# Kernel tuning notes

Measured on AMD Instinct MI355X. Metric: run time of the kernel, lower is better.

## Reference

```python
import jax, jax.numpy as jnp
import numpy as np


def _gcn_conv(x, W, b, src, dst, n):
    # PyG GCNConv: add self-loops, symmetric normalization deg^{-1/2} A deg^{-1/2},
    # linear transform, scatter-add aggregation, bias.
    h = x @ W  # [N, H]
    # degree including self-loop (count of dst occurrences + 1)
    deg = jnp.zeros((n,), h.dtype).at[dst].add(1.0) + 1.0
    dinv = jax.lax.rsqrt(deg)  # deg^{-1/2}
    edge_norm = (dinv[src] * dinv[dst])[:, None]  # [E, 1]
    agg = jax.ops.segment_sum(h[src] * edge_norm, dst, num_segments=n)  # [N, H]
    # self-loop contribution: norm = dinv[i]*dinv[i]
    return agg + h * (dinv * dinv)[:, None] + b


def setup_inputs() -> dict:
    N, E, F_IN, HID, OUT = 100000, 1600000, 128, 128, 64
    key = jax.random.key(0)
    ks = jax.random.split(key, 8)
    x = jax.random.normal(ks[0], (N, F_IN), dtype=jnp.float32)
    edge_index = jax.random.randint(ks[1], (2, E), 0, N, dtype=jnp.int32)
    s1 = 1.0 / np.sqrt(F_IN)
    s2 = 1.0 / np.sqrt(HID)
    W1 = jax.random.uniform(ks[2], (F_IN, HID), jnp.float32, -s1, s1)
    b1 = jax.random.uniform(ks[3], (HID,), jnp.float32, -s1, s1)
    W2 = jax.random.uniform(ks[4], (HID, HID), jnp.float32, -s2, s2)
    b2 = jax.random.uniform(ks[5], (HID,), jnp.float32, -s2, s2)
    W_out = jax.random.uniform(ks[6], (HID, OUT), jnp.float32, -s2, s2)
    b_out = jax.random.uniform(ks[7], (OUT,), jnp.float32, -s2, s2)
    return {"x": x, "edge_index": edge_index, "W1": W1, "b1": b1,
            "W2": W2, "b2": b2, "W_out": W_out, "b_out": b_out}


def reference(x, edge_index, W1, b1, W2, b2, W_out, b_out):
    n = x.shape[0]
    src, dst = edge_index[0], edge_index[1]
    h = _gcn_conv(x, W1, b1, src, dst, n)
    h = jax.nn.relu(h)
    # F.dropout(training=self.training): identity in eval mode
    h = _gcn_conv(h, W2, b2, src, dst, n)
    h = jax.nn.relu(h)
    logits = h @ W_out + b_out
    return jax.nn.log_softmax(logits, axis=1)
```

## Files before the change

### kernel.cpp

```cpp
#include <hip/hip_runtime.h>
#include <hip/hip_bf16.h>


#define FEAT 128
#define OUTF 64
#define BSH 7
#define BNODES (1 << BSH)
#define SCHUNK_SH 12
#define SCHUNK (1 << SCHUNK_SH)
#define NREP 8

typedef __attribute__((ext_vector_type(8))) short short8;
typedef __attribute__((ext_vector_type(4))) float f32x4;

__device__ __forceinline__ unsigned short bf16_rn(float f) {
    unsigned int u = __float_as_uint(f);
    u += 0x7FFFu + ((u >> 16) & 1u);
    return (unsigned short)(u >> 16);
}
__device__ __forceinline__ float bf16_lo(unsigned int u) { return __uint_as_float(u << 16); }
__device__ __forceinline__ float bf16_hi(unsigned int u) { return __uint_as_float(u & 0xFFFF0000u); }

__global__ __launch_bounds__(256) void bincount8_kernel(
        const int* __restrict__ dst, int* __restrict__ bcnt8, int E, int NB) {
    __shared__ int h[8192];
    int t = threadIdx.x;
    int nb8 = NB * NREP;
    for (int i = t; i < nb8; i += 256) h[i] = 0;
    __syncthreads();
    int stride = gridDim.x * 256;
    for (int e = blockIdx.x * 256 + t; e < E; e += stride) {
        int rep = (e >> SCHUNK_SH) & (NREP - 1);
        atomicAdd(&h[((dst[e] >> BSH) << 3) | rep], 1);
    }
    __syncthreads();
    for (int i = t; i < nb8; i += 256)
        if (h[i]) atomicAdd(&bcnt8[i], h[i]);
}

__global__ __launch_bounds__(1024) void bucket_scan8_kernel(
        const int* __restrict__ bcnt8, int* __restrict__ bcur8,
        int* __restrict__ bbase, int NB, int E) {
    int t = threadIdx.x;
    int nb8 = NB * NREP;
    int base = t * 8;
    int v[8];
    #pragma unroll
    for (int i = 0; i < 8; ++i) v[i] = (base + i < nb8) ? bcnt8[base + i] : 0;
    int local = 0;
    #pragma unroll
    for (int i = 0; i < 8; ++i) local += v[i];
    int lane = t & 63, wv = t >> 6;
    int x = local;
    #pragma unroll
    for (int o = 1; o < 64; o <<= 1) {
        int y = __shfl_up(x, o);
        if (lane >= o) x += y;
    }
    __shared__ int wsum[16];
    if (lane == 63) wsum[wv] = x;
    __syncthreads();
    int woff = 0;
    for (int i = 0; i < wv; ++i) woff += wsum[i];
    int run = woff + x - local;
    #pragma unroll
    for (int i = 0; i < 8; ++i) {
        int g = base + i;
        if (g < nb8) {
            bcur8[g] = run;
            if ((g & (NREP - 1)) == 0) bbase[g >> 3] = run;
        }
        run += v[i];
    }
    if (t == 0) bbase[NB] = E;
}

__global__ __launch_bounds__(256) void bin_scatter_kernel(
        const int* __restrict__ src, const int* __restrict__ dst,
        int* __restrict__ bcur8, unsigned int* __restrict__ staged,
        int E, int NB) {
    __shared__ int lcnt[1024];
    __shared__ int lbase[1024];
    int t = threadIdx.x;
    int rep = blockIdx.x & (NREP - 1);
    int e0 = blockIdx.x << SCHUNK_SH;
    int e1 = min(e0 + SCHUNK, E);
    for (int i = t; i < NB; i += 256) lcnt[i] = 0;
    __syncthreads();
    for (int e = e0 + t; e < e1; e += 256)
        atomicAdd(&lcnt[dst[e] >> BSH], 1);
    __syncthreads();
    for (int i = t; i < NB; i += 256) {
        int c = lcnt[i];
        lbase[i] = c ? atomicAdd(&bcur8[(i << 3) | rep], c) : 0;
        lcnt[i] = 0;
    }
    __syncthreads();
    for (int e = e0 + t; e < e1; e += 256) {
        int s = src[e], d = dst[e];
        int b = d >> BSH, dl = d & (BNODES - 1);
        int pos = lbase[b] + atomicAdd(&lcnt[b], 1);
        staged[pos] = (unsigned int)s | ((unsigned int)dl << 25);
    }
}

__global__ __launch_bounds__(256) void bucket_place_kernel(
        const unsigned int* __restrict__ staged, const int* __restrict__ bbase,
        int* __restrict__ row_ptr, float* __restrict__ dinv,
        int* __restrict__ csr_src, int N, int E) {
    int b = blockIdx.x;
    int t = threadIdx.x;
    int base = bbase[b], end = bbase[b + 1];
    __shared__ int cnt[BNODES];
    __shared__ int cur[BNODES];
    __shared__ int wsum2[2];
    if (t < BNODES) cnt[t] = 0;
    __syncthreads();
    for (int i = base + t; i < end; i += 256)
        atomicAdd(&cnt[staged[i] >> 25], 1);
    __syncthreads();

    bool act = t < BNODES;
    int v = act ? cnt[t] : 0;
    int lane = t & 63, wv = t >> 6;
    int x = v;
    #pragma unroll
    for (int o = 1; o < 64; o <<= 1) {
        int y = __shfl_up(x, o);
        if (lane >= o) x += y;
    }
    if (lane == 63 && wv == 0) wsum2[0] = x;
    __syncthreads();
    if (act) {
        int excl = x - v + (wv == 1 ? wsum2[0] : 0);
        int gnode = b * BNODES + t;
        int rp = base + excl;
        cur[t] = rp;
        if (gnode < N) {
            row_ptr[gnode] = rp;
            dinv[gnode] = rsqrtf((float)v + 1.0f);
        }
    }
    __syncthreads();
    for (int i = base + t; i < end; i += 256) {
        unsigned int u = staged[i];
        int dl = u >> 25;
        int p = atomicAdd(&cur[dl], 1);
        csr_src[p] = (int)(u & 0x1FFFFFFu);
    }
    if (b == 0 && t == 0) row_ptr[N] = E;
}

__global__ __launch_bounds__(256) void convw_kernel(
        const float* __restrict__ W1, const float* __restrict__ W2,
        const float* __restrict__ Wout,
        __hip_bfloat16* __restrict__ W1t, __hip_bfloat16* __restrict__ W2t,
        __hip_bfloat16* __restrict__ WoutT) {
    int idx = blockIdx.x * 256 + threadIdx.x;
    if (idx < 2 * FEAT * FEAT) {
        int which = idx >> 14;
        int r = idx & (FEAT * FEAT - 1);
        int n = r >> 7, k = r & 127;
        const float* W = which ? W2 : W1;
        unsigned short* Wt = (unsigned short*)(which ? W2t : W1t);
        Wt[r] = bf16_rn(W[k * FEAT + n]);
    } else if (idx < 2 * FEAT * FEAT + OUTF * FEAT) {
        int r = idx - 2 * FEAT * FEAT;
        int n = r >> 7, k = r & 127;
        ((unsigned short*)WoutT)[r] = bf16_rn(Wout[k * OUTF + n]);
    }
}

template <bool IN_FP32>
__global__ __launch_bounds__(256) void mfma_gemm_kernel(
        const void* __restrict__ Xv, const __hip_bfloat16* __restrict__ Wt,
        const float* __restrict__ dinv, __hip_bfloat16* __restrict__ Y, int N) {
    __shared__ short Ws[FEAT][136];
    int t = threadIdx.x;
    for (int i = t; i < FEAT * 16; i += 256) {
        int n = i >> 4, c = i & 15;
        *(uint4*)&Ws[n][c * 8] = *(const uint4*)((const unsigned short*)Wt + n * FEAT + c * 8);
    }
    __syncthreads();

    int wave = t >> 6, lane = t & 63;
    int m = lane & 15, quad = lane >> 4;
    int rbase = (blockIdx.x * 4 + wave) * 16;
    if (rbase >= N) return;
    int row = rbase + m;
    bool rok = row < N;

    f32x4 acc[8];
    #pragma unroll
    for (int nt = 0; nt < 8; ++nt) acc[nt] = (f32x4){0.f, 0.f, 0.f, 0.f};

    #pragma unroll
    for (int ks = 0; ks < 4; ++ks) {
        short8 a;
        if (IN_FP32) {
            const float* X = (const float*)Xv;
            float xs[8];
            if (rok) {
                float4 x0 = *(const float4*)(X + (size_t)row * FEAT + ks * 32 + quad * 8);
                float4 x1 = *(const float4*)(X + (size_t)row * FEAT + ks * 32 + quad * 8 + 4);
                xs[0] = x0.x; xs[1] = x0.y; xs[2] = x0.z; xs[3] = x0.w;
                xs[4] = x1.x; xs[5] = x1.y; xs[6] = x1.z; xs[7] = x1.w;
            } else {
                #pragma unroll
                for (int j = 0; j < 8; ++j) xs[j] = 0.f;
            }
            #pragma unroll
            for (int j = 0; j < 8; ++j) a[j] = (short)bf16_rn(xs[j]);
        } else {
            const unsigned short* X = (const unsigned short*)Xv;
            if (rok)
                a = *(const short8*)(X + (size_t)row * FEAT + ks * 32 + quad * 8);
            else {
                #pragma unroll
                for (int j = 0; j < 8; ++j) a[j] = 0;
            }
        }
        #pragma unroll
        for (int nt = 0; nt < 8; ++nt) {
            short8 bfr = *(const short8*)&Ws[nt * 16 + m][ks * 32 + quad * 8];
            acc[nt] = __builtin_amdgcn_mfma_f32_16x16x32_bf16(a, bfr, acc[nt], 0, 0, 0);
        }
    }

    float dr[4];
    #pragma unroll
    for (int r = 0; r < 4; ++r) {
        int ro = rbase + quad * 4 + r;
        dr[r] = (ro < N) ? dinv[ro] : 0.f;
    }
    unsigned short* Yo = (unsigned short*)Y;
    #pragma unroll
    for (int nt = 0; nt < 8; ++nt) {
        #pragma unroll
        for (int r = 0; r < 4; ++r) {
            int ro = rbase + quad * 4 + r;
            if (ro < N)
                Yo[(size_t)ro * FEAT + nt * 16 + m] = bf16_rn(acc[nt][r] * dr[r]);
        }
    }
}

__global__ __launch_bounds__(256) void gather_kernel(
        const int* __restrict__ row_ptr, const int* __restrict__ csr_src,
        const float* __restrict__ dinv, const __hip_bfloat16* __restrict__ Hs,
        const float* __restrict__ bias, __hip_bfloat16* __restrict__ A, int N) {
    int node = blockIdx.x * 4 + (threadIdx.x >> 6);
    if (node >= N) return;
    int lane = threadIdx.x & 63;
    const unsigned int* H2 = (const unsigned int*)Hs;
    float ax = 0.f, ay = 0.f;

    int j = row_ptr[node], end = row_ptr[node + 1];
    for (; j + 8 <= end; j += 8) {
        int s0 = csr_src[j + 0], s1 = csr_src[j + 1];
        int s2 = csr_src[j + 2], s3 = csr_src[j + 3];
        int s4 = csr_src[j + 4], s5 = csr_src[j + 5];
        int s6 = csr_src[j + 6], s7 = csr_src[j + 7];
        unsigned int u0 = H2[(size_t)s0 * 64 + lane];
        unsigned int u1 = H2[(size_t)s1 * 64 + lane];
        unsigned int u2 = H2[(size_t)s2 * 64 + lane];
        unsigned int u3 = H2[(size_t)s3 * 64 + lane];
        unsigned int u4 = H2[(size_t)s4 * 64 + lane];
        unsigned int u5 = H2[(size_t)s5 * 64 + lane];
        unsigned int u6 = H2[(size_t)s6 * 64 + lane];
        unsigned int u7 = H2[(size_t)s7 * 64 + lane];
        ax += bf16_lo(u0) + bf16_lo(u1) + bf16_lo(u2) + bf16_lo(u3)
            + bf16_lo(u4) + bf16_lo(u5) + bf16_lo(u6) + bf16_lo(u7);
        ay += bf16_hi(u0) + bf16_hi(u1) + bf16_hi(u2) + bf16_hi(u3)
            + bf16_hi(u4) + bf16_hi(u5) + bf16_hi(u6) + bf16_hi(u7);
    }
    for (; j < end; ++j) {
        int s = csr_src[j];
        unsigned int u = H2[(size_t)s * 64 + lane];
        ax += bf16_lo(u);
        ay += bf16_hi(u);
    }
    unsigned int hu = H2[(size_t)node * 64 + lane];
    ax += bf16_lo(hu);
    ay += bf16_hi(hu);
    float di = dinv[node];
    float2 b2 = ((const float2*)bias)[lane];
    ax = fmaxf(di * ax + b2.x, 0.f);
    ay = fmaxf(di * ay + b2.y, 0.f);
    ((unsigned int*)A)[(size_t)node * 64 + lane] =
        (unsigned int)bf16_rn(ax) | ((unsigned int)bf16_rn(ay) << 16);
}

__global__ __launch_bounds__(256) void final_mfma_kernel(
        const __hip_bfloat16* __restrict__ H, const __hip_bfloat16* __restrict__ WoutT,
        const float* __restrict__ bout, float* __restrict__ out, int N) {
    __shared__ short Ws[OUTF][136];
    int t = threadIdx.x;
    for (int i = t; i < OUTF * 16; i += 256) {
        int n = i >> 4, c = i & 15;
        *(uint4*)&Ws[n][c * 8] = *(const uint4*)((const unsigned short*)WoutT + n * FEAT + c * 8);
    }
    __syncthreads();

    int wave = t >> 6, lane = t & 63;
    int m = lane & 15, quad = lane >> 4;
    int rbase = blockIdx.x * 64 + wave * 16;
    if (rbase >= N) return;
    int row = rbase + m;
    bool rok = row < N;

    f32x4 acc[4];
    #pragma unroll
    for (int nt = 0; nt < 4; ++nt) acc[nt] = (f32x4){0.f, 0.f, 0.f, 0.f};

    const unsigned short* Hu = (const unsigned short*)H;
    #pragma unroll
    for (int ks = 0; ks < 4; ++ks) {
        short8 a;
        if (rok)
            a = *(const short8*)(Hu + (size_t)row * FEAT + ks * 32 + quad * 8);
        else {
            #pragma unroll
            for (int j = 0; j < 8; ++j) a[j] = 0;
        }
        #pragma unroll
        for (int nt = 0; nt < 4; ++nt) {
            short8 bfr = *(const short8*)&Ws[nt * 16 + m][ks * 32 + quad * 8];
            acc[nt] = __builtin_amdgcn_mfma_f32_16x16x32_bf16(a, bfr, acc[nt], 0, 0, 0);
        }
    }

    float bj[4];
    #pragma unroll
    for (int nt = 0; nt < 4; ++nt) bj[nt] = bout[nt * 16 + m];

    #pragma unroll
    for (int r = 0; r < 4; ++r) {
        int ro = rbase + quad * 4 + r;
        if (ro >= N) continue;
        float v0 = acc[0][r] + bj[0];
        float v1 = acc[1][r] + bj[1];
        float v2 = acc[2][r] + bj[2];
        float v3 = acc[3][r] + bj[3];
        float mx = fmaxf(fmaxf(v0, v1), fmaxf(v2, v3));
        #pragma unroll
        for (int o = 1; o <= 8; o <<= 1) mx = fmaxf(mx, __shfl_xor(mx, o));
        float s = __expf(v0 - mx) + __expf(v1 - mx) + __expf(v2 - mx) + __expf(v3 - mx);
        #pragma unroll
        for (int o = 1; o <= 8; o <<= 1) s += __shfl_xor(s, o);
        float ls = mx + __logf(s);
        float* op = out + (size_t)ro * OUTF + m;
        op[0]  = v0 - ls;
        op[16] = v1 - ls;
        op[32] = v2 - ls;
        op[48] = v3 - ls;
    }
}

extern "C" void kernel_launch(void* const* d_in, const int* in_sizes, int n_in,
                              void* d_out, int out_size, void* d_ws, size_t ws_size,
                              hipStream_t stream) {
    const float* x    = (const float*)d_in[0];
    const int*   ei   = (const int*)  d_in[1];
    const float* W1   = (const float*)d_in[2];
    const float* b1   = (const float*)d_in[3];
    const float* W2   = (const float*)d_in[4];
    const float* b2   = (const float*)d_in[5];
    const float* Wout = (const float*)d_in[6];
    const float* bout = (const float*)d_in[7];
    float* out = (float*)d_out;

    int N = in_sizes[0] / FEAT;
    int E = in_sizes[1] / 2;
    const int* srcp = ei;
    const int* dstp = ei + E;
    int NB = (N + BNODES - 1) >> BSH;

    char* ws = (char*)d_ws;
    __hip_bfloat16* Bh   = (__hip_bfloat16*)ws;
    __hip_bfloat16* Ba   = Bh + (size_t)N * FEAT;
    __hip_bfloat16* W1t  = Ba + (size_t)N * FEAT;
    __hip_bfloat16* W2t  = W1t + FEAT * FEAT;
    __hip_bfloat16* WoutT = W2t + FEAT * FEAT;
    float* dinv    = (float*)(WoutT + OUTF * FEAT);
    int*   rowp    = (int*)(dinv + N);
    int*   bcnt8   = rowp + N + 1;
    int*   bcur8   = bcnt8 + 8192;
    int*   bbase   = bcur8 + 8192;
    unsigned int* staged = (unsigned int*)(bbase + 1032);
    int*   csrsrc  = (int*)(staged + E);

    hipMemsetAsync(bcnt8, 0, (size_t)NB * NREP * sizeof(int), stream);
    bincount8_kernel<<<256, 256, 0, stream>>>(dstp, bcnt8, E, NB);
    bucket_scan8_kernel<<<1, 1024, 0, stream>>>(bcnt8, bcur8, bbase, NB, E);
    bin_scatter_kernel<<<(E + SCHUNK - 1) / SCHUNK, 256, 0, stream>>>(
        srcp, dstp, bcur8, staged, E, NB);
    bucket_place_kernel<<<NB, 256, 0, stream>>>(staged, bbase, rowp, dinv, csrsrc, N, E);
    convw_kernel<<<(2 * FEAT * FEAT + OUTF * FEAT + 255) / 256, 256, 0, stream>>>(
        W1, W2, Wout, W1t, W2t, WoutT);

    int ggrid = (N + 63) / 64;
    int agrid = (N + 3) / 4;

    mfma_gemm_kernel<true><<<ggrid, 256, 0, stream>>>(x, W1t, dinv, Bh, N);
    gather_kernel<<<agrid, 256, 0, stream>>>(rowp, csrsrc, dinv, Bh, b1, Ba, N);

    mfma_gemm_kernel<false><<<ggrid, 256, 0, stream>>>(Ba, W2t, dinv, Bh, N);
    gather_kernel<<<agrid, 256, 0, stream>>>(rowp, csrsrc, dinv, Bh, b2, Ba, N);

    final_mfma_kernel<<<(N + 63) / 64, 256, 0, stream>>>(Ba, WoutT, bout, out, N);
}
```

Measured before the change: 371.1 us.

## Fuse histogram, scan and weight conversion into one kernel; cache edges in LDS

Merges the bincount, single-block scan and weight-conversion kernels into one launch. The scan is done by the last histogram block, found through an atomic done counter and threadfence. The aim is to cut two kernel launches and their serialization gaps. bin_scatter now caches dst in LDS so it is read from global memory once, and bucket_place caches each staged bucket in LDS so it is read once when the bucket fits. The larger LDS use may lower occupancy, and the scan now runs on only 256 threads.

```diff
diff --git a/kernel.cpp b/kernel.cpp
--- a/kernel.cpp
+++ b/kernel.cpp
@@ -9,6 +9,7 @@
 #define SCHUNK_SH 12
 #define SCHUNK (1 << SCHUNK_SH)
 #define NREP 8
+#define NHIST 256
 
 typedef __attribute__((ext_vector_type(8))) short short8;
 typedef __attribute__((ext_vector_type(4))) float f32x4;
@@ -21,35 +22,65 @@
 __device__ __forceinline__ float bf16_lo(unsigned int u) { return __uint_as_float(u << 16); }
 __device__ __forceinline__ float bf16_hi(unsigned int u) { return __uint_as_float(u & 0xFFFF0000u); }
 
-__global__ __launch_bounds__(256) void bincount8_kernel(
-        const int* __restrict__ dst, int* __restrict__ bcnt8, int E, int NB) {
+__global__ __launch_bounds__(256) void build1_kernel(
+        const int* __restrict__ dst, int* __restrict__ bcnt8,
+        int* __restrict__ done, int* __restrict__ bcur8, int* __restrict__ bbase,
+        int E, int NB,
+        const float* __restrict__ W1, const float* __restrict__ W2,
+        const float* __restrict__ Wout,
+        __hip_bfloat16* __restrict__ W1t, __hip_bfloat16* __restrict__ W2t,
+        __hip_bfloat16* __restrict__ WoutT) {
+    int t = threadIdx.x;
+    int bid = blockIdx.x;
+
+    if (bid >= NHIST) {
+        int idx = (bid - NHIST) * 256 + t;
+        if (idx < 2 * FEAT * FEAT) {
+            int which = idx >> 14;
+            int r = idx & (FEAT * FEAT - 1);
+            int n = r >> 7, k = r & 127;
+            const float* W = which ? W2 : W1;
+            unsigned short* Wt = (unsigned short*)(which ? W2t : W1t);
+            Wt[r] = bf16_rn(W[k * FEAT + n]);
+        } else if (idx < 2 * FEAT * FEAT + OUTF * FEAT) {
+            int r = idx - 2 * FEAT * FEAT;
+            int n = r >> 7, k = r & 127;
+            ((unsigned short*)WoutT)[r] = bf16_rn(Wout[k * OUTF + n]);
+        }
+        return;
+    }
+
     __shared__ int h[8192];
-    int t = threadIdx.x;
     int nb8 = NB * NREP;
     for (int i = t; i < nb8; i += 256) h[i] = 0;
     __syncthreads();
-    int stride = gridDim.x * 256;
-    for (int e = blockIdx.x * 256 + t; e < E; e += stride) {
+    int stride = NHIST * 256;
+    for (int e = bid * 256 + t; e < E; e += stride) {
         int rep = (e >> SCHUNK_SH) & (NREP - 1);
         atomicAdd(&h[((dst[e] >> BSH) << 3) | rep], 1);
     }
     __syncthreads();
     for (int i = t; i < nb8; i += 256)
         if (h[i]) atomicAdd(&bcnt8[i], h[i]);
-}
-
-__global__ __launch_bounds__(1024) void bucket_scan8_kernel(
-        const int* __restrict__ bcnt8, int* __restrict__ bcur8,
-        int* __restrict__ bbase, int NB, int E) {
-    int t = threadIdx.x;
-    int nb8 = NB * NREP;
-    int base = t * 8;
-    int v[8];
-    #pragma unroll
-    for (int i = 0; i < 8; ++i) v[i] = (base + i < nb8) ? bcnt8[base + i] : 0;
+
+    __shared__ int amLast;
+    __threadfence();
+    __syncthreads();
+    if (t == 0) amLast = (atomicAdd(done, 1) == NHIST - 1);
+    __syncthreads();
+    if (!amLast) return;
+    __threadfence();
+
+    int per = 32;
+    int base = t * per;
+    int v[32];
     int local = 0;
     #pragma unroll
-    for (int i = 0; i < 8; ++i) local += v[i];
+    for (int i = 0; i < 32; ++i) {
+        int g = base + i;
+        v[i] = (g < nb8) ? bcnt8[g] : 0;
+        local += v[i];
+    }
     int lane = t & 63, wv = t >> 6;
     int x = local;
     #pragma unroll
@@ -57,14 +88,14 @@
         int y = __shfl_up(x, o);
         if (lane >= o) x += y;
     }
-    __shared__ int wsum[16];
+    __shared__ int wsum[4];
     if (lane == 63) wsum[wv] = x;
     __syncthreads();
     int woff = 0;
     for (int i = 0; i < wv; ++i) woff += wsum[i];
     int run = woff + x - local;
     #pragma unroll
-    for (int i = 0; i < 8; ++i) {
+    for (int i = 0; i < 32; ++i) {
         int g = base + i;
         if (g < nb8) {
             bcur8[g] = run;
@@ -81,14 +112,19 @@
         int E, int NB) {
     __shared__ int lcnt[1024];
     __shared__ int lbase[1024];
+    __shared__ int dstb[SCHUNK];
     int t = threadIdx.x;
     int rep = blockIdx.x & (NREP - 1);
     int e0 = blockIdx.x << SCHUNK_SH;
     int e1 = min(e0 + SCHUNK, E);
+    int len = e1 - e0;
     for (int i = t; i < NB; i += 256) lcnt[i] = 0;
     __syncthreads();
-    for (int e = e0 + t; e < e1; e += 256)
-        atomicAdd(&lcnt[dst[e] >> BSH], 1);
+    for (int li = t; li < len; li += 256) {
+        int d = dst[e0 + li];
+        dstb[li] = d;
+        atomicAdd(&lcnt[d >> BSH], 1);
+    }
     __syncthreads();
     for (int i = t; i < NB; i += 256) {
         int c = lcnt[i];
@@ -96,8 +132,8 @@
         lcnt[i] = 0;
     }
     __syncthreads();
-    for (int e = e0 + t; e < e1; e += 256) {
-        int s = src[e], d = dst[e];
+    for (int li = t; li < len; li += 256) {
+        int s = src[e0 + li], d = dstb[li];
         int b = d >> BSH, dl = d & (BNODES - 1);
         int pos = lbase[b] + atomicAdd(&lcnt[b], 1);
         staged[pos] = (unsigned int)s | ((unsigned int)dl << 25);
@@ -111,13 +147,24 @@
     int b = blockIdx.x;
     int t = threadIdx.x;
     int base = bbase[b], end = bbase[b + 1];
+    int len = end - base;
+    __shared__ unsigned int buf[4096];
     __shared__ int cnt[BNODES];
     __shared__ int cur[BNODES];
     __shared__ int wsum2[2];
+    bool fits = len <= 4096;
     if (t < BNODES) cnt[t] = 0;
     __syncthreads();
-    for (int i = base + t; i < end; i += 256)
-        atomicAdd(&cnt[staged[i] >> 25], 1);
+    if (fits) {
+        for (int i = t; i < len; i += 256) {
+            unsigned int u = staged[base + i];
+            buf[i] = u;
+            atomicAdd(&cnt[u >> 25], 1);
+        }
+    } else {
+        for (int i = base + t; i < end; i += 256)
+            atomicAdd(&cnt[staged[i] >> 25], 1);
+    }
     __syncthreads();
 
     bool act = t < BNODES;
@@ -142,33 +189,22 @@
         }
     }
     __syncthreads();
-    for (int i = base + t; i < end; i += 256) {
-        unsigned int u = staged[i];
-        int dl = u >> 25;
-        int p = atomicAdd(&cur[dl], 1);
-        csr_src[p] = (int)(u & 0x1FFFFFFu);
+    if (fits) {
+        for (int i = t; i < len; i += 256) {
+            unsigned int u = buf[i];
+            int dl = u >> 25;
+            int p = atomicAdd(&cur[dl], 1);
+            csr_src[p] = (int)(u & 0x1FFFFFFu);
+        }
+    } else {
+        for (int i = base + t; i < end; i += 256) {
+            unsigned int u = staged[i];
+            int dl = u >> 25;
+            int p = atomicAdd(&cur[dl], 1);
+            csr_src[p] = (int)(u & 0x1FFFFFFu);
+        }
     }
     if (b == 0 && t == 0) row_ptr[N] = E;
-}
-
-__global__ __launch_bounds__(256) void convw_kernel(
-        const float* __restrict__ W1, const float* __restrict__ W2,
-        const float* __restrict__ Wout,
-        __hip_bfloat16* __restrict__ W1t, __hip_bfloat16* __restrict__ W2t,
-        __hip_bfloat16* __restrict__ WoutT) {
-    int idx = blockIdx.x * 256 + threadIdx.x;
-    if (idx < 2 * FEAT * FEAT) {
-        int which = idx >> 14;
-        int r = idx & (FEAT * FEAT - 1);
-        int n = r >> 7, k = r & 127;
-        const float* W = which ? W2 : W1;
-        unsigned short* Wt = (unsigned short*)(which ? W2t : W1t);
-        Wt[r] = bf16_rn(W[k * FEAT + n]);
-    } else if (idx < 2 * FEAT * FEAT + OUTF * FEAT) {
-        int r = idx - 2 * FEAT * FEAT;
-        int n = r >> 7, k = r & 127;
-        ((unsigned short*)WoutT)[r] = bf16_rn(Wout[k * OUTF + n]);
-    }
 }
 
 template <bool IN_FP32>
@@ -385,19 +421,20 @@
     float* dinv    = (float*)(WoutT + OUTF * FEAT);
     int*   rowp    = (int*)(dinv + N);
     int*   bcnt8   = rowp + N + 1;
-    int*   bcur8   = bcnt8 + 8192;
+    int*   done    = bcnt8 + 8192;
+    int*   bcur8   = done + 1;
     int*   bbase   = bcur8 + 8192;
     unsigned int* staged = (unsigned int*)(bbase + 1032);
     int*   csrsrc  = (int*)(staged + E);
 
-    hipMemsetAsync(bcnt8, 0, (size_t)NB * NREP * sizeof(int), stream);
-    bincount8_kernel<<<256, 256, 0, stream>>>(dstp, bcnt8, E, NB);
-    bucket_scan8_kernel<<<1, 1024, 0, stream>>>(bcnt8, bcur8, bbase, NB, E);
+    hipMemsetAsync(bcnt8, 0, (size_t)(8192 + 1) * sizeof(int), stream);
+
+    int convw_blocks = (2 * FEAT * FEAT + OUTF * FEAT + 255) / 256;
+    build1_kernel<<<NHIST + convw_blocks, 256, 0, stream>>>(
+        dstp, bcnt8, done, bcur8, bbase, E, NB, W1, W2, Wout, W1t, W2t, WoutT);
     bin_scatter_kernel<<<(E + SCHUNK - 1) / SCHUNK, 256, 0, stream>>>(
         srcp, dstp, bcur8, staged, E, NB);
     bucket_place_kernel<<<NB, 256, 0, stream>>>(staged, bbase, rowp, dinv, csrsrc, N, E);
-    convw_kernel<<<(2 * FEAT * FEAT + OUTF * FEAT + 255) / 256, 256, 0, stream>>>(
-        W1, W2, Wout, W1t, W2t, WoutT);
 
     int ggrid = (N + 63) / 64;
     int agrid = (N + 3) / 4;
```

Result: slower. 380.8 us (+2.6%).
